# Kernel optimization log

Hardware: AMD Instinct MI355X
Metric: run time of the kernel (lower is better)

Reference implementation:

```python
import jax, jax.numpy as jnp
import numpy as np

B, S, H, D, M = 4, 512, 768, 24, 96
OUT_HID = 2 * max(128, H // 2)  # 768

def setup_inputs() -> dict:
    key = jax.random.key(0)
    ks = jax.random.split(key, 10)
    g = lambda k, shp, s=0.02: (jax.random.normal(k, shp, jnp.float32) * s)
    return {
        'H_j': jax.random.normal(ks[0], (B, S, H), jnp.float32),
        'H_i': jax.random.normal(ks[1], (B, S, H), jnp.float32),
        'attn_mask': jnp.ones((B, S), jnp.float32),
        'p_j_w': g(ks[2], (D, H)),
        'p_i_w': g(ks[3], (D, H)),
        's_w1': g(ks[4], (M, 4 * D)),
        's_b1': jnp.zeros((M,), jnp.float32),
        's_w2': g(ks[5], (1, M)),
        's_b2': jnp.zeros((1,), jnp.float32),
        'v_w1': g(ks[6], (OUT_HID, 3 * H)),
        'v_b1': jnp.zeros((OUT_HID,), jnp.float32),
        'v_w2': g(ks[7], (H, OUT_HID)),
        'v_b2': jnp.zeros((H,), jnp.float32),
        'alpha': jnp.asarray(0.05, jnp.float32),
    }

def reference(H_j, H_i, attn_mask, p_j_w, p_i_w, s_w1, s_b1, s_w2, s_b2,
              v_w1, v_b1, v_w2, v_b2, alpha):
    # Projections: [B,S,D]
    Zj = H_j @ p_j_w.T
    Zi = H_i @ p_i_w.T
    # score_mlp layer1 on concat([Zj_pair, Zi_pair, hadam, |diff|]) ==
    # sum of the 4 block-matmuls (block-split of W1 over the concat axis).
    Wa, Wb, Wc, Wd = jnp.split(s_w1, 4, axis=1)        # each [M, D]
    Zj_p = Zj[:, :, None, :]                            # [B,S,1,D]
    Zi_p = Zi[:, None, :, :]                            # [B,1,S,D]
    hid = (jnp.einsum('bsd,md->bsm', Zj, Wa)[:, :, None, :]
           + jnp.einsum('btd,md->btm', Zi, Wb)[:, None, :, :]
           + jnp.einsum('bstd,md->bstm', Zj_p * Zi_p, Wc)
           + jnp.einsum('bstd,md->bstm', jnp.abs(Zj_p - Zi_p), Wd)
           + s_b1)                                      # [B,S,S,M]
    logits = jnp.einsum('bstm,om->bst', jax.nn.relu(hid), s_w2)[..., :] + s_b2[0]  # [B,S,S]
    neg = jnp.finfo(logits.dtype).min
    logits = logits + (1.0 - attn_mask)[:, None, :] * neg  # mask over keys
    probs = jax.nn.softmax(logits, axis=-1)
    ctx = jnp.einsum('bst,bth->bsh', probs, H_i)           # [B,S,H]
    msg_in = jnp.concatenate([ctx, H_j, ctx * H_j], axis=-1)  # concat_hadam: [B,S,3H]
    msg = jax.nn.relu(msg_in @ v_w1.T + v_b1) @ v_w2.T + v_b2
    return alpha * msg  # dropout is identity in eval mode
```

## Files before the change

kernel.cpp:

```cpp
#include <hip/hip_runtime.h>
#include <hip/hip_bf16.h>
#include <math.h>

#define BB 4
#define SS 512
#define HH 768
#define DD 24
#define MM 96
#define OH 768
#define K3H 2304

typedef unsigned short u16;
typedef unsigned int u32;
typedef short bf16x8 __attribute__((ext_vector_type(8)));
typedef float f32x4 __attribute__((ext_vector_type(4)));
typedef u16 u16x4 __attribute__((ext_vector_type(4)));

#define OFF_A     0
#define F32_END   (OFF_A + BB*SS*MM)
#define MB_MSGIN  0
#define MB_H1     (MB_MSGIN + BB*SS*K3H)
#define MB_W1     (MB_H1    + BB*SS*OH)
#define MB_W2     (MB_W1    + OH*K3H)
#define MB_PROBS  (MB_W2    + OH*HH)
#define MB_HIT    (MB_PROBS + BB*SS*SS)
#define MB_ZJP    (MB_HIT   + BB*HH*SS)
#define MB_ZIP    (MB_ZJP   + BB*SS*32)
#define MB_WM     (MB_ZIP   + BB*SS*32)

__device__ inline u16 f2bf(float x) {
    union { float f; u32 u; } v; v.f = x;
    u32 r = v.u + 0x7fffu + ((v.u >> 16) & 1u);
    return (u16)(r >> 16);
}
__device__ inline u32 pk2bf(float lo, float hi) {
    return ((__float_as_uint(lo) + 0x8000u) >> 16) |
           ((__float_as_uint(hi) + 0x8000u) & 0xffff0000u);
}
__device__ inline void unpack8(bf16x8 v, float* f) {
    const u32* d = (const u32*)&v;
    #pragma unroll
    for (int i = 0; i < 4; ++i) {
        f[2*i]   = __uint_as_float(d[i] << 16);
        f[2*i+1] = __uint_as_float(d[i] & 0xffff0000u);
    }
}
__device__ inline void gl_lds16(const u16* g, u16* l) {
    __builtin_amdgcn_global_load_lds(
        (const __attribute__((address_space(1))) void*)g,
        (__attribute__((address_space(3))) void*)l, 16, 0, 0);
}

__global__ __launch_bounds__(256) void k_zproj(
    const float* __restrict__ Hj, const float* __restrict__ Hi,
    const float* __restrict__ pjw, const float* __restrict__ piw,
    const float* __restrict__ sw1, const float* __restrict__ sb1,
    u16* __restrict__ Zjp, u16* __restrict__ Zip, float* __restrict__ A)
{
    int bs = blockIdx.x;
    __shared__ float hj[HH], hi[HH], zj[DD], zi[DD];
    int tid = threadIdx.x;
    for (int i = tid; i < HH; i += 256) {
        hj[i] = Hj[(size_t)bs*HH + i];
        hi[i] = Hi[(size_t)bs*HH + i];
    }
    __syncthreads();
    int wid = tid >> 6, lane = tid & 63;
    for (int o = wid; o < 2*DD; o += 4) {
        int isJ = (o < DD); int d = isJ ? o : o - DD;
        const float* w = (isJ ? pjw : piw) + (size_t)d * HH;
        const float* x = isJ ? hj : hi;
        float acc = 0.f;
        #pragma unroll
        for (int k = 0; k < HH/64; ++k) { int h = lane + 64*k; acc = fmaf(x[h], w[h], acc); }
        #pragma unroll
        for (int off = 32; off > 0; off >>= 1) acc += __shfl_down(acc, off);
        if (lane == 0) { if (isJ) zj[d] = acc; else zi[d] = acc; }
    }
    __syncthreads();
    if (tid < 32)      Zjp[(size_t)bs*32 + tid] = (tid < DD) ? f2bf(zj[tid]) : (u16)0;
    else if (tid < 64) { int c = tid - 32; Zip[(size_t)bs*32 + c] = (c < DD) ? f2bf(zi[c]) : (u16)0; }
    if (tid < MM) {
        float acc = sb1[tid];
        #pragma unroll
        for (int d = 0; d < DD; ++d) acc = fmaf(zj[d], sw1[tid*96 + d], acc);
        A[(size_t)bs*MM + tid] = acc;
    }
}

__global__ __launch_bounds__(256) void k_prep(
    const float* __restrict__ sw1, u16* __restrict__ Wm)
{
    for (int i = threadIdx.x; i < MM*96; i += 256) {
        int m = i / 96, k = i % 96;
        float v = 0.f;
        if (k < 24)                 v = sw1[m*96 + 48 + k];
        else if (k >= 32 && k < 56) v = sw1[m*96 + 72 + (k - 32)];
        else if (k >= 64 && k < 88) v = sw1[m*96 + 24 + (k - 64)];
        Wm[i] = f2bf(v);
    }
}

__global__ __launch_bounds__(256) void k_pair_mfma(
    const u16* __restrict__ Zjp, const u16* __restrict__ Zip,
    const float* __restrict__ A, const u16* __restrict__ Wm,
    const float* __restrict__ sw2, const float* __restrict__ mask,
    u16* __restrict__ probsb)
{
    int blk = blockIdx.x; int b = blk >> 7; int s0 = (blk & 127) * 4;
    int tid = threadIdx.x, wave = tid >> 6, lane = tid & 63;
    int q = lane >> 4, l16 = lane & 15;
    __shared__ float logits[SS];
    __shared__ float wpart[8];

    bf16x8 af[6][3];
    #pragma unroll
    for (int mt = 0; mt < 6; ++mt)
        #pragma unroll
        for (int ks = 0; ks < 3; ++ks)
            af[mt][ks] = *(const bf16x8*)&Wm[(mt*16 + l16)*96 + ks*32 + q*8];
    float w2v[6][4];
    #pragma unroll
    for (int mt = 0; mt < 6; ++mt)
        #pragma unroll
        for (int r = 0; r < 4; ++r) w2v[mt][r] = sw2[mt*16 + q*4 + r];

    const float NEGF = -3.4028234663852886e38f;

    for (int si = 0; si < 4; ++si) {
        int s = s0 + si; int bs = b*SS + s;
        bf16x8 zjf = *(const bf16x8*)&Zjp[(size_t)bs*32 + q*8];
        float zj[8]; unpack8(zjf, zj);
        #pragma unroll
        for (int mt = 0; mt < 6; ++mt) {
            u32 aval = (u32)f2bf(A[(size_t)bs*MM + mt*16 + l16]);
            u32* dw = (u32*)&af[mt][2];
            dw[0] = (q == 3) ? aval : dw[0];
        }

        for (int tt = wave; tt < 32; tt += 4) {
            int t0 = tt*16;
            bf16x8 zif = *(const bf16x8*)&Zip[((size_t)(b*SS) + t0 + l16)*32 + q*8];
            float zi[8]; unpack8(zif, zi);
            bf16x8 b2 = zif;
            { u32* dw = (u32*)&b2; dw[0] = (q == 3) ? 0x3F80u : dw[0]; }
            bf16x8 b0, b1;
            {
                u32* p0 = (u32*)&b0; u32* p1 = (u32*)&b1;
                #pragma unroll
                for (int i = 0; i < 4; ++i) {
                    p0[i] = pk2bf(zj[2*i]*zi[2*i], zj[2*i+1]*zi[2*i+1]);
                    p1[i] = pk2bf(fabsf(zj[2*i]-zi[2*i]), fabsf(zj[2*i+1]-zi[2*i+1]));
                }
            }
            f32x4 acc[6] = {};
            #pragma unroll
            for (int mt = 0; mt < 6; ++mt) {
                acc[mt] = __builtin_amdgcn_mfma_f32_16x16x32_bf16(af[mt][0], b0, acc[mt], 0,0,0);
                acc[mt] = __builtin_amdgcn_mfma_f32_16x16x32_bf16(af[mt][1], b1, acc[mt], 0,0,0);
                acc[mt] = __builtin_amdgcn_mfma_f32_16x16x32_bf16(af[mt][2], b2, acc[mt], 0,0,0);
            }
            float p = 0.f;
            #pragma unroll
            for (int mt = 0; mt < 6; ++mt)
                #pragma unroll
                for (int r = 0; r < 4; ++r)
                    p = fmaf(fmaxf(acc[mt][r], 0.f), w2v[mt][r], p);
            p += __shfl_xor(p, 16);
            p += __shfl_xor(p, 32);
            if (lane < 16) logits[t0 + lane] = p;
        }
        __syncthreads();
        float l0 = logits[tid]       + (1.f - mask[b*SS + tid])       * NEGF;
        float l1 = logits[tid + 256] + (1.f - mask[b*SS + tid + 256]) * NEGF;
        float mloc = fmaxf(l0, l1);
        #pragma unroll
        for (int off = 32; off > 0; off >>= 1) mloc = fmaxf(mloc, __shfl_xor(mloc, off));
        if (lane == 0) wpart[wave] = mloc;
        __syncthreads();
        float mx = fmaxf(fmaxf(wpart[0], wpart[1]), fmaxf(wpart[2], wpart[3]));
        float e0 = __expf(l0 - mx), e1 = __expf(l1 - mx);
        float sloc = e0 + e1;
        #pragma unroll
        for (int off = 32; off > 0; off >>= 1) sloc += __shfl_xor(sloc, off);
        if (lane == 0) wpart[4 + wave] = sloc;
        __syncthreads();
        float inv = 1.f / (wpart[4] + wpart[5] + wpart[6] + wpart[7]);
        probsb[(size_t)bs*SS + tid]       = f2bf(e0 * inv);
        probsb[(size_t)bs*SS + tid + 256] = f2bf(e1 * inv);
        __syncthreads();
    }
}

__global__ __launch_bounds__(256) void k_hit(
    const float* __restrict__ Hi, u16* __restrict__ HiTb)
{
    int b = blockIdx.z; int t0 = blockIdx.x * 32; int h0 = blockIdx.y * 32;
    __shared__ float tile[32][33];
    int tx = threadIdx.x & 31, ty = threadIdx.x >> 5;
    for (int i = ty; i < 32; i += 8)
        tile[i][tx] = Hi[((size_t)(b*SS) + t0 + i)*HH + h0 + tx];
    __syncthreads();
    for (int i = ty; i < 32; i += 8)
        HiTb[((size_t)b*HH + h0 + i)*SS + t0 + tx] = f2bf(tile[tx][i]);
}

__global__ __launch_bounds__(256) void k_cast_bf(
    const float* __restrict__ in, u16* __restrict__ out, int n)
{
    int i = (blockIdx.x*256 + threadIdx.x) * 8;
    if (i >= n) return;
    float4 a = *(const float4*)&in[i];
    float4 b = *(const float4*)&in[i+4];
    u16x4 lo = { f2bf(a.x), f2bf(a.y), f2bf(a.z), f2bf(a.w) };
    u16x4 hi = { f2bf(b.x), f2bf(b.y), f2bf(b.z), f2bf(b.w) };
    *(u16x4*)&out[i]   = lo;
    *(u16x4*)&out[i+4] = hi;
}

__global__ __launch_bounds__(256) void k_ctx_mfma(
    const u16* __restrict__ probsb, const u16* __restrict__ HiTb,
    const float* __restrict__ Hj, u16* __restrict__ msginb)
{
    int b = blockIdx.z;
    int h0 = blockIdx.x * 64;
    int s0 = blockIdx.y * 64;
    int tid = threadIdx.x;
    __shared__ __align__(16) u16 As[64*32];
    __shared__ __align__(16) u16 Bs[64*32];
    int row = tid >> 2, cs = tid & 3;
    int gchunk = cs ^ ((row >> 1) & 3);
    int wave = tid >> 6, lane = tid & 63;
    int wr = (wave >> 1) * 32, wc = (wave & 1) * 32;
    int q = lane >> 4, l16 = lane & 15;
    int sA = (l16 >> 1) & 3;
    f32x4 acc00 = {}, acc01 = {}, acc10 = {}, acc11 = {};
    const u16* ag = probsb + ((size_t)(b*SS) + s0 + row)*SS + gchunk*8;
    const u16* bg = HiTb + ((size_t)b*HH + h0 + row)*SS + gchunk*8;
    u16* lA = As + tid*8;
    u16* lB = Bs + tid*8;
    for (int k0 = 0; k0 < SS; k0 += 32) {
        gl_lds16(ag + k0, lA);
        gl_lds16(bg + k0, lB);
        __syncthreads();
        bf16x8 a0 = *(const bf16x8*)&As[(wr      + l16)*32 + (q^sA)*8];
        bf16x8 a1 = *(const bf16x8*)&As[(wr + 16 + l16)*32 + (q^sA)*8];
        bf16x8 b0 = *(const bf16x8*)&Bs[(wc      + l16)*32 + (q^sA)*8];
        bf16x8 b1 = *(const bf16x8*)&Bs[(wc + 16 + l16)*32 + (q^sA)*8];
        acc00 = __builtin_amdgcn_mfma_f32_16x16x32_bf16(a0, b0, acc00, 0,0,0);
        acc01 = __builtin_amdgcn_mfma_f32_16x16x32_bf16(a0, b1, acc01, 0,0,0);
        acc10 = __builtin_amdgcn_mfma_f32_16x16x32_bf16(a1, b0, acc10, 0,0,0);
        acc11 = __builtin_amdgcn_mfma_f32_16x16x32_bf16(a1, b1, acc11, 0,0,0);
        __syncthreads();
    }
    #pragma unroll
    for (int rt = 0; rt < 2; ++rt) {
        #pragma unroll
        for (int ct = 0; ct < 2; ++ct) {
            const f32x4* ac = rt ? (ct ? &acc11 : &acc10) : (ct ? &acc01 : &acc00);
            int h = h0 + wc + ct*16 + l16;
            #pragma unroll
            for (int r = 0; r < 4; ++r) {
                int s = s0 + wr + rt*16 + q*4 + r;
                float v = (*ac)[r];
                float hj = Hj[((size_t)(b*SS) + s)*HH + h];
                u16* mb = msginb + (size_t)(b*SS + s)*K3H + h;
                mb[0]    = f2bf(v);
                mb[HH]   = f2bf(hj);
                mb[2*HH] = f2bf(v * hj);
            }
        }
    }
}

__global__ __launch_bounds__(256) void k_mfma_gemm1(
    const u16* __restrict__ Abf, const u16* __restrict__ Bbf,
    const float* __restrict__ bias, u16* __restrict__ Cbf)
{
    int o0 = blockIdx.x * 64;
    int n0 = blockIdx.y * 64;
    int tid = threadIdx.x;
    __shared__ __align__(16) u16 As[64*32];
    __shared__ __align__(16) u16 Bs[64*32];
    int row = tid >> 2, cs = tid & 3;
    int gchunk = cs ^ ((row >> 1) & 3);
    int wave = tid >> 6, lane = tid & 63;
    int wr = (wave >> 1) * 32, wc = (wave & 1) * 32;
    int q = lane >> 4, l16 = lane & 15;
    int sA = (l16 >> 1) & 3;
    f32x4 acc00 = {}, acc01 = {}, acc10 = {}, acc11 = {};
    const u16* ag = Abf + (size_t)(n0 + row)*K3H + gchunk*8;
    const u16* bg = Bbf + (size_t)(o0 + row)*K3H + gchunk*8;
    u16* lA = As + tid*8;
    u16* lB = Bs + tid*8;
    for (int k0 = 0; k0 < K3H; k0 += 32) {
        gl_lds16(ag + k0, lA);
        gl_lds16(bg + k0, lB);
        __syncthreads();
        bf16x8 a0 = *(const bf16x8*)&As[(wr      + l16)*32 + (q^sA)*8];
        bf16x8 a1 = *(const bf16x8*)&As[(wr + 16 + l16)*32 + (q^sA)*8];
        bf16x8 b0 = *(const bf16x8*)&Bs[(wc      + l16)*32 + (q^sA)*8];
        bf16x8 b1 = *(const bf16x8*)&Bs[(wc + 16 + l16)*32 + (q^sA)*8];
        acc00 = __builtin_amdgcn_mfma_f32_16x16x32_bf16(a0, b0, acc00, 0,0,0);
        acc01 = __builtin_amdgcn_mfma_f32_16x16x32_bf16(a0, b1, acc01, 0,0,0);
        acc10 = __builtin_amdgcn_mfma_f32_16x16x32_bf16(a1, b0, acc10, 0,0,0);
        acc11 = __builtin_amdgcn_mfma_f32_16x16x32_bf16(a1, b1, acc11, 0,0,0);
        __syncthreads();
    }
    #pragma unroll
    for (int rt = 0; rt < 2; ++rt) {
        #pragma unroll
        for (int ct = 0; ct < 2; ++ct) {
            const f32x4* ac = rt ? (ct ? &acc11 : &acc10) : (ct ? &acc01 : &acc00);
            int o = o0 + wc + ct*16 + l16;
            float bv = bias[o];
            #pragma unroll
            for (int r = 0; r < 4; ++r) {
                int m = n0 + wr + rt*16 + q*4 + r;
                Cbf[(size_t)m*OH + o] = f2bf(fmaxf((*ac)[r] + bv, 0.f));
            }
        }
    }
}

__global__ __launch_bounds__(256) void k_mfma_gemm2(
    const u16* __restrict__ Abf, const u16* __restrict__ Bbf,
    const float* __restrict__ bias, const float* __restrict__ alpha,
    float* __restrict__ out)
{
    int o0 = blockIdx.x * 64;
    int n0 = blockIdx.y * 64;
    int tid = threadIdx.x;
    __shared__ __align__(16) u16 As[64*32];
    __shared__ __align__(16) u16 Bs[64*32];
    int row = tid >> 2, cs = tid & 3;
    int gchunk = cs ^ ((row >> 1) & 3);
    int wave = tid >> 6, lane = tid & 63;
    int wr = (wave >> 1) * 32, wc = (wave & 1) * 32;
    int q = lane >> 4, l16 = lane & 15;
    int sA = (l16 >> 1) & 3;
    f32x4 acc00 = {}, acc01 = {}, acc10 = {}, acc11 = {};
    const u16* ag = Abf + (size_t)(n0 + row)*OH + gchunk*8;
    const u16* bg = Bbf + (size_t)(o0 + row)*OH + gchunk*8;
    u16* lA = As + tid*8;
    u16* lB = Bs + tid*8;
    for (int k0 = 0; k0 < OH; k0 += 32) {
        gl_lds16(ag + k0, lA);
        gl_lds16(bg + k0, lB);
        __syncthreads();
        bf16x8 a0 = *(const bf16x8*)&As[(wr      + l16)*32 + (q^sA)*8];
        bf16x8 a1 = *(const bf16x8*)&As[(wr + 16 + l16)*32 + (q^sA)*8];
        bf16x8 b0 = *(const bf16x8*)&Bs[(wc      + l16)*32 + (q^sA)*8];
        bf16x8 b1 = *(const bf16x8*)&Bs[(wc + 16 + l16)*32 + (q^sA)*8];
        acc00 = __builtin_amdgcn_mfma_f32_16x16x32_bf16(a0, b0, acc00, 0,0,0);
        acc01 = __builtin_amdgcn_mfma_f32_16x16x32_bf16(a0, b1, acc01, 0,0,0);
        acc10 = __builtin_amdgcn_mfma_f32_16x16x32_bf16(a1, b0, acc10, 0,0,0);
        acc11 = __builtin_amdgcn_mfma_f32_16x16x32_bf16(a1, b1, acc11, 0,0,0);
        __syncthreads();
    }
    float al = alpha[0];
    #pragma unroll
    for (int rt = 0; rt < 2; ++rt) {
        #pragma unroll
        for (int ct = 0; ct < 2; ++ct) {
            const f32x4* ac = rt ? (ct ? &acc11 : &acc10) : (ct ? &acc01 : &acc00);
            int o = o0 + wc + ct*16 + l16;
            float bv = bias[o];
            #pragma unroll
            for (int r = 0; r < 4; ++r) {
                int m = n0 + wr + rt*16 + q*4 + r;
                out[(size_t)m*HH + o] = al * ((*ac)[r] + bv);
            }
        }
    }
}

extern "C" void kernel_launch(void* const* d_in, const int* in_sizes, int n_in,
                              void* d_out, int out_size, void* d_ws, size_t ws_size,
                              hipStream_t stream) {
    const float* Hj    = (const float*)d_in[0];
    const float* Hi    = (const float*)d_in[1];
    const float* amask = (const float*)d_in[2];
    const float* pjw   = (const float*)d_in[3];
    const float* piw   = (const float*)d_in[4];
    const float* sw1   = (const float*)d_in[5];
    const float* sb1   = (const float*)d_in[6];
    const float* sw2   = (const float*)d_in[7];
    const float* sb2   = (const float*)d_in[8];
    const float* vw1   = (const float*)d_in[9];
    const float* vb1   = (const float*)d_in[10];
    const float* vw2   = (const float*)d_in[11];
    const float* vb2   = (const float*)d_in[12];
    const float* alpha = (const float*)d_in[13];
    float* out = (float*)d_out;
    (void)sb2;

    float* ws   = (float*)d_ws;
    float* A    = ws + OFF_A;
    u16* bfbase = (u16*)(ws + F32_END);
    u16* msginb = bfbase + MB_MSGIN;
    u16* h1b    = bfbase + MB_H1;
    u16* w1b    = bfbase + MB_W1;
    u16* w2b    = bfbase + MB_W2;
    u16* probsb = bfbase + MB_PROBS;
    u16* hitb   = bfbase + MB_HIT;
    u16* zjp    = bfbase + MB_ZJP;
    u16* zip    = bfbase + MB_ZIP;
    u16* wm     = bfbase + MB_WM;

    k_zproj<<<BB*SS, 256, 0, stream>>>(Hj, Hi, pjw, piw, sw1, sb1, zjp, zip, A);
    k_prep<<<1, 256, 0, stream>>>(sw1, wm);
    k_cast_bf<<<(OH*K3H/8 + 255)/256, 256, 0, stream>>>(vw1, w1b, OH*K3H);
    k_cast_bf<<<(HH*OH/8 + 255)/256, 256, 0, stream>>>(vw2, w2b, HH*OH);
    k_hit<<<dim3(SS/32, HH/32, BB), 256, 0, stream>>>(Hi, hitb);
    k_pair_mfma<<<BB*SS/4, 256, 0, stream>>>(zjp, zip, A, wm, sw2, amask, probsb);
    k_ctx_mfma<<<dim3(HH/64, SS/64, BB), 256, 0, stream>>>(probsb, hitb, Hj, msginb);
    k_mfma_gemm1<<<dim3(OH/64, BB*SS/64), 256, 0, stream>>>(msginb, w1b, vb1, h1b);
    k_mfma_gemm2<<<dim3(HH/64, BB*SS/64), 256, 0, stream>>>(h1b, w2b, vb2, alpha, out);
}
```

Baseline: 220.9 us.

## Fold Zj into pair-MLP weights, stage Zi in LDS, merge weight-prep kernels

The pair-scoring kernel folds the Hadamard term into the weight operand per query row: Wc*zj + Wb becomes one fragment, so each 16-key tile needs two MFMAs instead of three. The B operand reuses zi directly. Each block now handles 2 query rows with 2 waves per row, and stages the whole Zi panel for the batch in swizzled LDS, avoiding repeated global loads. Softmax now runs in one wave per row with no block-level reductions. The three weight-cast/prep launches merge into one kernel to cut launch overhead. In exchange, precision changes slightly because the folded weights are rounded to bf16, and there is 32KB of LDS per block, which may limit occupancy.

```diff
diff --git a/kernel.cpp b/kernel.cpp
--- a/kernel.cpp
+++ b/kernel.cpp
@@ -88,17 +88,34 @@
     }
 }
 
-__global__ __launch_bounds__(256) void k_prep(
-    const float* __restrict__ sw1, u16* __restrict__ Wm)
-{
-    for (int i = threadIdx.x; i < MM*96; i += 256) {
-        int m = i / 96, k = i % 96;
-        float v = 0.f;
-        if (k < 24)                 v = sw1[m*96 + 48 + k];
-        else if (k >= 32 && k < 56) v = sw1[m*96 + 72 + (k - 32)];
-        else if (k >= 64 && k < 88) v = sw1[m*96 + 24 + (k - 64)];
-        Wm[i] = f2bf(v);
-    }
+__global__ __launch_bounds__(256) void k_wprep(
+    const float* __restrict__ sw1, const float* __restrict__ vw1,
+    const float* __restrict__ vw2,
+    u16* __restrict__ Wm, u16* __restrict__ w1b, u16* __restrict__ w2b)
+{
+    int bx = blockIdx.x;
+    if (bx == 0) {
+        for (int i = threadIdx.x; i < MM*96; i += 256) {
+            int m = i / 96, k = i % 96;
+            float v = 0.f;
+            if (k < 24)                 v = sw1[m*96 + 48 + k];
+            else if (k >= 32 && k < 56) v = sw1[m*96 + 72 + (k - 32)];
+            else if (k >= 64 && k < 88) v = sw1[m*96 + 24 + (k - 64)];
+            Wm[i] = f2bf(v);
+        }
+        return;
+    }
+    int idx = bx - 1;
+    const float* src; u16* dst;
+    if (idx < 864) { src = vw1; dst = w1b; }
+    else           { idx -= 864; src = vw2; dst = w2b; }
+    int i = (idx*256 + threadIdx.x) * 8;
+    float4 a = *(const float4*)&src[i];
+    float4 c = *(const float4*)&src[i+4];
+    u16x4 lo = { f2bf(a.x), f2bf(a.y), f2bf(a.z), f2bf(a.w) };
+    u16x4 hi = { f2bf(c.x), f2bf(c.y), f2bf(c.z), f2bf(c.w) };
+    *(u16x4*)&dst[i]   = lo;
+    *(u16x4*)&dst[i+4] = hi;
 }
 
 __global__ __launch_bounds__(256) void k_pair_mfma(
@@ -107,88 +124,107 @@
     const float* __restrict__ sw2, const float* __restrict__ mask,
     u16* __restrict__ probsb)
 {
-    int blk = blockIdx.x; int b = blk >> 7; int s0 = (blk & 127) * 4;
+    int blk = blockIdx.x; int b = blk >> 8; int s0 = (blk & 255) * 2;
     int tid = threadIdx.x, wave = tid >> 6, lane = tid & 63;
     int q = lane >> 4, l16 = lane & 15;
-    __shared__ float logits[SS];
-    __shared__ float wpart[8];
-
-    bf16x8 af[6][3];
+    int si = wave & 1, half = wave >> 1;
+    int s = s0 + si, bs = b*SS + s;
+    __shared__ __align__(16) u16 ZiS[SS*32];
+    __shared__ float logits[2][SS];
+
+    {
+        const u16* zb = Zip + (size_t)b*SS*32;
+        #pragma unroll
+        for (int p = 0; p < 8; ++p) {
+            int idx = p*256 + tid;
+            int t = idx >> 2, c = idx & 3;
+            int g = c ^ ((t + (t >> 2)) & 3);
+            gl_lds16(zb + t*32 + g*8, ZiS + idx*8);
+        }
+    }
+
+    bf16x8 zjf = *(const bf16x8*)&Zjp[(size_t)bs*32 + q*8];
+    float zj[8]; unpack8(zjf, zj);
+    bf16x8 afc[6], afd[6];
+    #pragma unroll
+    for (int mt = 0; mt < 6; ++mt) {
+        const u16* wrow = &Wm[(mt*16 + l16)*96];
+        bf16x8 wcf = *(const bf16x8*)&wrow[q*8];
+        afd[mt]    = *(const bf16x8*)&wrow[32 + q*8];
+        bf16x8 wbf = *(const bf16x8*)&wrow[64 + q*8];
+        float fc[8], fb[8];
+        unpack8(wcf, fc); unpack8(wbf, fb);
+        u32 aval = (u32)f2bf(A[(size_t)bs*MM + mt*16 + l16]);
+        union { u32 d[4]; bf16x8 v; } pk;
+        #pragma unroll
+        for (int i = 0; i < 4; ++i)
+            pk.d[i] = pk2bf(fmaf(fc[2*i], zj[2*i], fb[2*i]),
+                            fmaf(fc[2*i+1], zj[2*i+1], fb[2*i+1]));
+        pk.d[0] = (q == 3) ? aval : pk.d[0];
+        afc[mt] = pk.v;
+    }
+    float w2v[6][4];
     #pragma unroll
     for (int mt = 0; mt < 6; ++mt)
         #pragma unroll
-        for (int ks = 0; ks < 3; ++ks)
-            af[mt][ks] = *(const bf16x8*)&Wm[(mt*16 + l16)*96 + ks*32 + q*8];
-    float w2v[6][4];
-    #pragma unroll
-    for (int mt = 0; mt < 6; ++mt)
-        #pragma unroll
         for (int r = 0; r < 4; ++r) w2v[mt][r] = sw2[mt*16 + q*4 + r];
 
-    const float NEGF = -3.4028234663852886e38f;
-
-    for (int si = 0; si < 4; ++si) {
-        int s = s0 + si; int bs = b*SS + s;
-        bf16x8 zjf = *(const bf16x8*)&Zjp[(size_t)bs*32 + q*8];
-        float zj[8]; unpack8(zjf, zj);
+    __syncthreads();
+
+    for (int k = 0; k < 16; ++k) {
+        int t0 = (half*16 + k) * 16;
+        int trow = t0 + l16;
+        int sw = q ^ ((trow + (trow >> 2)) & 3);
+        bf16x8 zif = *(const bf16x8*)&ZiS[trow*32 + sw*8];
+        float zi[8]; unpack8(zif, zi);
+        union { u32 d[4]; bf16x8 v; } b1, b2;
+        #pragma unroll
+        for (int i = 0; i < 4; ++i)
+            b1.d[i] = pk2bf(fabsf(zj[2*i] - zi[2*i]), fabsf(zj[2*i+1] - zi[2*i+1]));
+        b2.v = zif;
+        b2.d[0] = (q == 3) ? 0x3F80u : b2.d[0];
+        f32x4 acc[6];
         #pragma unroll
         for (int mt = 0; mt < 6; ++mt) {
-            u32 aval = (u32)f2bf(A[(size_t)bs*MM + mt*16 + l16]);
-            u32* dw = (u32*)&af[mt][2];
-            dw[0] = (q == 3) ? aval : dw[0];
-        }
-
-        for (int tt = wave; tt < 32; tt += 4) {
-            int t0 = tt*16;
-            bf16x8 zif = *(const bf16x8*)&Zip[((size_t)(b*SS) + t0 + l16)*32 + q*8];
-            float zi[8]; unpack8(zif, zi);
-            bf16x8 b2 = zif;
-            { u32* dw = (u32*)&b2; dw[0] = (q == 3) ? 0x3F80u : dw[0]; }
-            bf16x8 b0, b1;
-            {
-                u32* p0 = (u32*)&b0; u32* p1 = (u32*)&b1;
-                #pragma unroll
-                for (int i = 0; i < 4; ++i) {
-                    p0[i] = pk2bf(zj[2*i]*zi[2*i], zj[2*i+1]*zi[2*i+1]);
-                    p1[i] = pk2bf(fabsf(zj[2*i]-zi[2*i]), fabsf(zj[2*i+1]-zi[2*i+1]));
-                }
-            }
-            f32x4 acc[6] = {};
+            f32x4 a = {};
+            a = __builtin_amdgcn_mfma_f32_16x16x32_bf16(afc[mt], b2.v, a, 0,0,0);
+            a = __builtin_amdgcn_mfma_f32_16x16x32_bf16(afd[mt], b1.v, a, 0,0,0);
+            acc[mt] = a;
+        }
+        float p = 0.f;
+        #pragma unroll
+        for (int mt = 0; mt < 6; ++mt)
             #pragma unroll
-            for (int mt = 0; mt < 6; ++mt) {
-                acc[mt] = __builtin_amdgcn_mfma_f32_16x16x32_bf16(af[mt][0], b0, acc[mt], 0,0,0);
-                acc[mt] = __builtin_amdgcn_mfma_f32_16x16x32_bf16(af[mt][1], b1, acc[mt], 0,0,0);
-                acc[mt] = __builtin_amdgcn_mfma_f32_16x16x32_bf16(af[mt][2], b2, acc[mt], 0,0,0);
-            }
-            float p = 0.f;
-            #pragma unroll
-            for (int mt = 0; mt < 6; ++mt)
-                #pragma unroll
-                for (int r = 0; r < 4; ++r)
-                    p = fmaf(fmaxf(acc[mt][r], 0.f), w2v[mt][r], p);
-            p += __shfl_xor(p, 16);
-            p += __shfl_xor(p, 32);
-            if (lane < 16) logits[t0 + lane] = p;
-        }
-        __syncthreads();
-        float l0 = logits[tid]       + (1.f - mask[b*SS + tid])       * NEGF;
-        float l1 = logits[tid + 256] + (1.f - mask[b*SS + tid + 256]) * NEGF;
-        float mloc = fmaxf(l0, l1);
-        #pragma unroll
-        for (int off = 32; off > 0; off >>= 1) mloc = fmaxf(mloc, __shfl_xor(mloc, off));
-        if (lane == 0) wpart[wave] = mloc;
-        __syncthreads();
-        float mx = fmaxf(fmaxf(wpart[0], wpart[1]), fmaxf(wpart[2], wpart[3]));
-        float e0 = __expf(l0 - mx), e1 = __expf(l1 - mx);
-        float sloc = e0 + e1;
-        #pragma unroll
-        for (int off = 32; off > 0; off >>= 1) sloc += __shfl_xor(sloc, off);
-        if (lane == 0) wpart[4 + wave] = sloc;
-        __syncthreads();
-        float inv = 1.f / (wpart[4] + wpart[5] + wpart[6] + wpart[7]);
-        probsb[(size_t)bs*SS + tid]       = f2bf(e0 * inv);
-        probsb[(size_t)bs*SS + tid + 256] = f2bf(e1 * inv);
-        __syncthreads();
+            for (int r = 0; r < 4; ++r)
+                p = fmaf(fmaxf(acc[mt][r], 0.f), w2v[mt][r], p);
+        p += __shfl_xor(p, 16);
+        p += __shfl_xor(p, 32);
+        if (lane < 16) logits[si][t0 + lane] = p;
+    }
+    __syncthreads();
+
+    if (wave < 2) {
+        const float NEGF = -3.4028234663852886e38f;
+        int bss = b*SS + s0 + wave;
+        float l[8], e[8];
+        float mx = -INFINITY;
+        #pragma unroll
+        for (int i = 0; i < 8; ++i) {
+            int idx = lane + i*64;
+            l[i] = logits[wave][idx] + (1.f - mask[b*SS + idx]) * NEGF;
+            mx = fmaxf(mx, l[i]);
+        }
+        #pragma unroll
+        for (int off = 32; off > 0; off >>= 1) mx = fmaxf(mx, __shfl_xor(mx, off));
+        float sum = 0.f;
+        #pragma unroll
+        for (int i = 0; i < 8; ++i) { e[i] = __expf(l[i] - mx); sum += e[i]; }
+        #pragma unroll
+        for (int off = 32; off > 0; off >>= 1) sum += __shfl_xor(sum, off);
+        float inv = 1.f / sum;
+        #pragma unroll
+        for (int i = 0; i < 8; ++i)
+            probsb[(size_t)bss*SS + lane + i*64] = f2bf(e[i] * inv);
     }
 }
 
@@ -203,19 +239,6 @@
     __syncthreads();
     for (int i = ty; i < 32; i += 8)
         HiTb[((size_t)b*HH + h0 + i)*SS + t0 + tx] = f2bf(tile[tx][i]);
-}
-
-__global__ __launch_bounds__(256) void k_cast_bf(
-    const float* __restrict__ in, u16* __restrict__ out, int n)
-{
-    int i = (blockIdx.x*256 + threadIdx.x) * 8;
-    if (i >= n) return;
-    float4 a = *(const float4*)&in[i];
-    float4 b = *(const float4*)&in[i+4];
-    u16x4 lo = { f2bf(a.x), f2bf(a.y), f2bf(a.z), f2bf(a.w) };
-    u16x4 hi = { f2bf(b.x), f2bf(b.y), f2bf(b.z), f2bf(b.w) };
-    *(u16x4*)&out[i]   = lo;
-    *(u16x4*)&out[i+4] = hi;
 }
 
 __global__ __launch_bounds__(256) void k_ctx_mfma(
@@ -409,11 +432,9 @@
     u16* wm     = bfbase + MB_WM;
 
     k_zproj<<<BB*SS, 256, 0, stream>>>(Hj, Hi, pjw, piw, sw1, sb1, zjp, zip, A);
-    k_prep<<<1, 256, 0, stream>>>(sw1, wm);
-    k_cast_bf<<<(OH*K3H/8 + 255)/256, 256, 0, stream>>>(vw1, w1b, OH*K3H);
-    k_cast_bf<<<(HH*OH/8 + 255)/256, 256, 0, stream>>>(vw2, w2b, HH*OH);
+    k_wprep<<<1 + 864 + 288, 256, 0, stream>>>(sw1, vw1, vw2, wm, w1b, w2b);
     k_hit<<<dim3(SS/32, HH/32, BB), 256, 0, stream>>>(Hi, hitb);
-    k_pair_mfma<<<BB*SS/4, 256, 0, stream>>>(zjp, zip, A, wm, sw2, amask, probsb);
+    k_pair_mfma<<<BB*SS/2, 256, 0, stream>>>(zjp, zip, A, wm, sw2, amask, probsb);
     k_ctx_mfma<<<dim3(HH/64, SS/64, BB), 256, 0, stream>>>(probsb, hitb, Hj, msginb);
     k_mfma_gemm1<<<dim3(OH/64, BB*SS/64), 256, 0, stream>>>(msginb, w1b, vb1, h1b);
     k_mfma_gemm2<<<dim3(HH/64, BB*SS/64), 256, 0, stream>>>(h1b, w2b, vb2, alpha, out);
```

New measurement: 204.1 us. 7.6% less time.
